# Performance work log

Measured on AMD Instinct MI355X. Metric: run time of the kernel, lower is better.

Reference implementation:

```python
import jax, jax.numpy as jnp
import numpy as np

B, N, IN_DIM = 2, 2048, 1024
DIM, DEPTH, HEADS, DH = 512, 4, 8, 128
INNER = HEADS * DH  # 1024
MLP, NCLS = 1024, 2
EPS = 1e-5


def setup_inputs() -> dict:
    key = jax.random.key(0)
    ks = jax.random.split(key, 10)
    r = lambda k, shape: (jax.random.normal(k, shape, dtype=jnp.float32) * 0.02)
    return {
        "x": jax.random.normal(ks[0], (B, N, IN_DIM), dtype=jnp.float32),
        "mask": jnp.ones((B, N), dtype=jnp.float32),
        "proj_w": r(ks[1], (IN_DIM, DIM)),
        "proj_b": jnp.zeros((DIM,), jnp.float32),
        "cls_token": jax.random.normal(ks[2], (1, 1, DIM), dtype=jnp.float32),
        "ln1_g": jnp.ones((DEPTH, DIM), jnp.float32),
        "ln1_b": jnp.zeros((DEPTH, DIM), jnp.float32),
        "qkv_w": r(ks[3], (DEPTH, DIM, 3 * INNER)),
        "out_w": r(ks[4], (DEPTH, INNER, DIM)),
        "out_b": jnp.zeros((DEPTH, DIM), jnp.float32),
        "ln2_g": jnp.ones((DEPTH, DIM), jnp.float32),
        "ln2_b": jnp.zeros((DEPTH, DIM), jnp.float32),
        "ff_w1": r(ks[5], (DEPTH, DIM, MLP)),
        "ff_b1": jnp.zeros((DEPTH, MLP), jnp.float32),
        "ff_w2": r(ks[6], (DEPTH, MLP, DIM)),
        "ff_b2": jnp.zeros((DEPTH, DIM), jnp.float32),
        "norm_g": jnp.ones((DIM,), jnp.float32),
        "norm_b": jnp.zeros((DIM,), jnp.float32),
        "head_ln_g": jnp.ones((DIM,), jnp.float32),
        "head_ln_b": jnp.zeros((DIM,), jnp.float32),
        "head_w": r(ks[7], (DIM, NCLS)),
        "head_b": jnp.zeros((NCLS,), jnp.float32),
    }


def _ln(x, g, b):
    m = jnp.mean(x, axis=-1, keepdims=True)
    v = jnp.mean((x - m) ** 2, axis=-1, keepdims=True)
    return (x - m) * jax.lax.rsqrt(v + EPS) * g + b


def reference(x, mask, proj_w, proj_b, cls_token, ln1_g, ln1_b, qkv_w, out_w,
              out_b, ln2_g, ln2_b, ff_w1, ff_b1, ff_w2, ff_b2, norm_g, norm_b,
              head_ln_g, head_ln_b, head_w, head_b):
    b = x.shape[0]
    scale = DH ** -0.5
    # input projection + ReLU
    h = jax.nn.relu(x @ proj_w + proj_b)  # [b, n, dim]
    # prepend cls token; extend mask with a 1 for it
    cls = jnp.broadcast_to(cls_token, (b, 1, DIM))
    h = jnp.concatenate([cls, h], axis=1)  # [b, n+1, dim]
    m_full = jnp.concatenate([jnp.ones((b, 1), mask.dtype), mask], axis=1)
    keep = (m_full != 0)[:, None, None, :]  # [b,1,1,n+1]

    for l in range(DEPTH):  # NOTE: original blocks have NO residual connections
        hn = _ln(h, ln1_g[l], ln1_b[l])
        qkv = hn @ qkv_w[l]  # [b, n+1, 3*inner]
        q, k, v = jnp.split(qkv, 3, axis=-1)
        resh = lambda t: t.reshape(b, -1, HEADS, DH).transpose(0, 2, 1, 3)
        q, k, v = resh(q), resh(k), resh(v)  # [b, h, n+1, dh]
        dots = jnp.einsum('bhid,bhjd->bhij', q, k) * scale
        dots = jnp.where(keep, dots, -jnp.inf)
        attn = jax.nn.softmax(dots, axis=-1)
        o = jnp.einsum('bhij,bhjd->bhid', attn, v)
        o = o.transpose(0, 2, 1, 3).reshape(b, -1, INNER)
        h = o @ out_w[l] + out_b[l]  # attention out (no residual)
        hn = _ln(h, ln2_g[l], ln2_b[l])
        h = jax.nn.gelu(hn @ ff_w1[l] + ff_b1[l], approximate=False) @ ff_w2[l] + ff_b2[l]

    pooled = h[:, 0]  # cls pooling
    pooled = _ln(pooled, norm_g, norm_b)
    pooled = _ln(pooled, head_ln_g, head_ln_b)
    return pooled @ head_w + head_b  # [b, num_classes]
```

## Files before the change

### kernel.cpp

```cpp
#include <hip/hip_runtime.h>
#include <hip/hip_bf16.h>
#include <stdint.h>

#define B_      2
#define N_      2048
#define S_      2049
#define SP_     2176
#define MP_     (B_*SP_)
#define IN_DIM_ 1024
#define DIM_    512
#define HEADS_  8
#define DH_     128
#define INNER_  1024
#define MLP_    1024
#define DEPTH_  4
#define NKV_    (SP_/64)
#define NCHUNK_ 4
#define TPC_    9

typedef __bf16 bf16;
typedef __bf16 bf16x4 __attribute__((ext_vector_type(4)));
typedef __bf16 bf16x8 __attribute__((ext_vector_type(8)));
typedef float  f32x4  __attribute__((ext_vector_type(4)));

#define AS1 __attribute__((address_space(1)))
#define AS3 __attribute__((address_space(3)))
__device__ __forceinline__ void gload16(const bf16* g, bf16* l) {
    __builtin_amdgcn_global_load_lds((const AS1 void*)g, (AS3 void*)l, 16, 0, 0);
}

__global__ __launch_bounds__(256) void wconv_kernel(const float* __restrict__ src,
                                                    bf16* __restrict__ dst,
                                                    int K, int N)
{
    __shared__ float tile[32][33];
    size_t mo = (size_t)blockIdx.z * K * N;
    int n0 = blockIdx.x * 32, k0 = blockIdx.y * 32;
    int tx = threadIdx.x & 31, ty = threadIdx.x >> 5;
#pragma unroll
    for (int i = 0; i < 32; i += 8)
        tile[ty + i][tx] = src[mo + (size_t)(k0 + ty + i) * N + n0 + tx];
    __syncthreads();
#pragma unroll
    for (int i = 0; i < 32; i += 8)
        dst[mo + (size_t)(n0 + ty + i) * K + k0 + tx] = (bf16)tile[tx][ty + i];
}

__global__ __launch_bounds__(256) void xconv_kernel(const float* __restrict__ x,
                                                    bf16* __restrict__ xb)
{
    int idx = blockIdx.x * 256 + threadIdx.x;
    int row = idx >> 7;
    int c   = (idx & 127) * 8;
    int b = row / SP_, s = row - b * SP_;
    bf16x8 v;
    if (s >= 1 && s <= N_) {
        const float* src = x + (size_t)(b * N_ + s - 1) * IN_DIM_ + c;
#pragma unroll
        for (int i = 0; i < 8; ++i) v[i] = (bf16)src[i];
    } else {
#pragma unroll
        for (int i = 0; i < 8; ++i) v[i] = (bf16)0.f;
    }
    *(bf16x8*)&xb[(size_t)row * IN_DIM_ + c] = v;
}

__global__ __launch_bounds__(256) void mask_kernel(const float* __restrict__ mask,
                                                   float* __restrict__ pb)
{
    int j = blockIdx.x * 256 + threadIdx.x;
    int b = blockIdx.y;
    if (j >= SP_) return;
    float v;
    if (j == 0) v = 0.f;
    else if (j <= N_) v = (mask[(size_t)b * N_ + j - 1] != 0.f) ? 0.f : -1e30f;
    else v = -1e30f;
    pb[(size_t)b * SP_ + j] = v;
}

__global__ void cls_kernel(const float* __restrict__ cls, float* __restrict__ h)
{
    h[(size_t)(blockIdx.x * SP_) * DIM_ + threadIdx.x] = cls[threadIdx.x];
}

__global__ __launch_bounds__(256) void ln_kernel(const float* __restrict__ h,
                                                 const float* __restrict__ g,
                                                 const float* __restrict__ bta,
                                                 bf16* __restrict__ out)
{
    int row  = blockIdx.x * 4 + (threadIdx.x >> 6);
    int lane = threadIdx.x & 63;
    const float* x = h + (size_t)row * DIM_;
    float v[8]; float s = 0.f;
#pragma unroll
    for (int i = 0; i < 8; ++i) { v[i] = x[lane + 64 * i]; s += v[i]; }
#pragma unroll
    for (int o = 32; o; o >>= 1) s += __shfl_xor(s, o);
    float mean = s * (1.f / DIM_);
    float vs = 0.f;
#pragma unroll
    for (int i = 0; i < 8; ++i) { float d = v[i] - mean; vs += d * d; }
#pragma unroll
    for (int o = 32; o; o >>= 1) vs += __shfl_xor(vs, o);
    float rstd = rsqrtf(vs * (1.f / DIM_) + 1e-5f);
    bf16* orow = out + (size_t)row * DIM_;
#pragma unroll
    for (int i = 0; i < 8; ++i)
        orow[lane + 64 * i] = (bf16)((v[i] - mean) * rstd * g[lane + 64 * i] + bta[lane + 64 * i]);
}

template<int BM, int BN, int ACT, int OUTBF>
__global__ __launch_bounds__(256) void gemm_bt(const bf16* __restrict__ A,
                                               const bf16* __restrict__ Bt,
                                               const float* __restrict__ bias,
                                               void* __restrict__ Cp,
                                               int M, int N, int K)
{
    constexpr int MF = (BM == 128) ? 4 : ((BN == 128) ? 4 : 2);
    constexpr int NF = (BM == 128) ? 4 : 2;
    constexpr int AT = BM / 32, BT = BN / 32;
    __shared__ __align__(16) bf16 As[BM * 64];
    __shared__ __align__(16) bf16 Bs[BN * 64];
    const int tid  = threadIdx.x;
    const int wave = tid >> 6, lane = tid & 63;
    const int bm = blockIdx.x * BM, bn = blockIdx.y * BN;
    const int wr = (BM == 128) ? (wave >> 1) * 64 : ((BN == 64) ? (wave >> 1) * 32 : 0);
    const int wc = (BM == 128) ? (wave & 1) * 64 : ((BN == 64) ? (wave & 1) * 32 : wave * 32);
    const int fr = lane & 15, fk = (lane >> 4) * 8;
    const int gr = lane >> 3, gc = (lane & 7) * 8;

    f32x4 acc[MF][NF];
#pragma unroll
    for (int m = 0; m < MF; ++m)
#pragma unroll
        for (int n = 0; n < NF; ++n) acc[m][n] = (f32x4){0.f, 0.f, 0.f, 0.f};

    for (int k0 = 0; k0 < K; k0 += 64) {
#pragma unroll
        for (int t = 0; t < AT; ++t) {
            int chunk = wave * AT + t;
            int r = chunk * 8 + gr;
            gload16(&A[(size_t)(bm + r) * K + k0 + (gc ^ ((r & 7) << 3))], &As[chunk * 512]);
        }
#pragma unroll
        for (int t = 0; t < BT; ++t) {
            int chunk = wave * BT + t;
            int r = chunk * 8 + gr;
            gload16(&Bt[(size_t)(bn + r) * K + k0 + (gc ^ ((r & 7) << 3))], &Bs[chunk * 512]);
        }
        __syncthreads();
#pragma unroll
        for (int kk = 0; kk < 2; ++kk) {
            bf16x8 af[MF], bb[NF];
#pragma unroll
            for (int m = 0; m < MF; ++m) {
                int r = wr + m * 16 + fr;
                af[m] = *(const bf16x8*)&As[r * 64 + ((kk * 32 + fk) ^ ((r & 7) << 3))];
            }
#pragma unroll
            for (int n = 0; n < NF; ++n) {
                int r = wc + n * 16 + fr;
                bb[n] = *(const bf16x8*)&Bs[r * 64 + ((kk * 32 + fk) ^ ((r & 7) << 3))];
            }
#pragma unroll
            for (int m = 0; m < MF; ++m)
#pragma unroll
                for (int n = 0; n < NF; ++n)
                    acc[m][n] = __builtin_amdgcn_mfma_f32_16x16x32_bf16(af[m], bb[n], acc[m][n], 0, 0, 0);
        }
        __syncthreads();
    }

    const int fc = lane & 15, fr4 = (lane >> 4) * 4;
#pragma unroll
    for (int n = 0; n < NF; ++n) {
        int col = bn + wc + n * 16 + fc;
        float bv = bias ? bias[col] : 0.f;
#pragma unroll
        for (int m = 0; m < MF; ++m) {
#pragma unroll
            for (int j = 0; j < 4; ++j) {
                int row = bm + wr + m * 16 + fr4 + j;
                float v = acc[m][n][j] + bv;
                if (ACT == 1) v = fmaxf(v, 0.f);
                if (ACT == 2) v = 0.5f * v * (1.f + erff(v * 0.70710678118654752f));
                if (OUTBF) ((bf16*)Cp)[(size_t)row * N + col] = (bf16)v;
                else       ((float*)Cp)[(size_t)row * N + col] = v;
            }
        }
    }
}

__global__ __launch_bounds__(256)
__attribute__((amdgpu_num_vgpr(168)))
void attn_kernel(const bf16* __restrict__ qkv,
                 const float* __restrict__ pb,
                 bf16* __restrict__ o0,
                 bf16* __restrict__ o1,
                 bf16* __restrict__ o2,
                 bf16* __restrict__ o3,
                 float* __restrict__ mlbuf)
{
    __shared__ __align__(16) bf16 Ks[64 * 128];
    __shared__ __align__(16) bf16 Vt[128 * 64];
    __shared__ __align__(16) bf16 Ps[4][32 * 64];

    const int bh = blockIdx.x, b = bh >> 3, hh = bh & 7;
    const int q0 = blockIdx.y * 128;
    const int chunk = blockIdx.z;
    const int t0 = chunk * TPC_;
    const int t1 = (t0 + TPC_ < NKV_) ? t0 + TPC_ : NKV_;
    bf16* obuf = (chunk == 0) ? o0 : (chunk == 1) ? o1 : (chunk == 2) ? o2 : o3;

    const int tid = threadIdx.x, wave = tid >> 6, lane = tid & 63;
    const int fc = lane & 15, g = lane >> 4, g8 = g * 8, rr0 = g * 4;
    bf16* Pw = &Ps[wave][0];

    const bf16* qb  = qkv + (size_t)(b * SP_) * (3 * INNER_) + hh * DH_;
    const bf16* kb  = qb + INNER_;
    const bf16* vb  = qb + 2 * INNER_;
    const float* pbb = pb + (size_t)b * SP_;

    bf16x8 aq[2][4];
#pragma unroll
    for (int m = 0; m < 2; ++m)
#pragma unroll
        for (int kk = 0; kk < 4; ++kk)
            aq[m][kk] = *(const bf16x8*)&qb[(size_t)(q0 + wave * 32 + m * 16 + fc) * (3 * INNER_) + kk * 32 + g8];

    f32x4 accO[2][8];
#pragma unroll
    for (int m = 0; m < 2; ++m)
#pragma unroll
        for (int f = 0; f < 8; ++f) accO[m][f] = (f32x4){0.f, 0.f, 0.f, 0.f};
    float mrow[2] = {-3e38f, -3e38f};
    float lrow[2] = {0.f, 0.f};
    const float scale = 0.08838834764831845f;

    auto issueK = [&](int kt) {
        int j0 = kt * 64;
#pragma unroll
        for (int t = 0; t < 4; ++t) {
            int ck = wave * 4 + t;
            int r = ck * 4 + (lane >> 4);
            int cp = (lane & 15) * 8;
            gload16(&kb[(size_t)(j0 + r) * (3 * INNER_) + (cp ^ ((r & 15) << 3))], &Ks[ck * 512]);
        }
    };
    const int vquad = tid >> 4;
    const int vd8   = (tid & 15) * 8;
    bf16x8 vreg[4];
    auto issueV = [&](int kt) {
        int j0 = kt * 64;
#pragma unroll
        for (int i = 0; i < 4; ++i)
            vreg[i] = *(const bf16x8*)&vb[(size_t)(j0 + vquad * 4 + i) * (3 * INNER_) + vd8];
    };

    issueK(t0);
    issueV(t0);
    for (int kt = t0; kt < t1; ++kt) {
        int j0 = kt * 64;
        __syncthreads();
#pragma unroll
        for (int di = 0; di < 8; ++di) {
            int rd = vd8 + di;
            bf16x4 w = { vreg[0][di], vreg[1][di], vreg[2][di], vreg[3][di] };
            *(bf16x4*)&Vt[rd * 64 + ((vquad * 4) ^ ((((rd & 7) ^ ((rd >> 3) & 7))) << 3))] = w;
        }
        __syncthreads();
        if (kt + 1 < t1) issueV(kt + 1);

        f32x4 sf[2][4];
#pragma unroll
        for (int m = 0; m < 2; ++m)
#pragma unroll
            for (int f = 0; f < 4; ++f) sf[m][f] = (f32x4){0.f, 0.f, 0.f, 0.f};
        __builtin_amdgcn_s_setprio(1);
#pragma unroll
        for (int kk = 0; kk < 4; ++kk) {
            bf16x8 bk[4];
#pragma unroll
            for (int f = 0; f < 4; ++f) {
                int r = f * 16 + fc;
                bk[f] = *(const bf16x8*)&Ks[r * 128 + ((kk * 32 + g8) ^ ((r & 15) << 3))];
            }
#pragma unroll
            for (int m = 0; m < 2; ++m)
#pragma unroll
                for (int f = 0; f < 4; ++f)
                    sf[m][f] = __builtin_amdgcn_mfma_f32_16x16x32_bf16(bk[f], aq[m][kk], sf[m][f], 0, 0, 0);
        }
        __builtin_amdgcn_s_setprio(0);
        __syncthreads();
        if (kt + 1 < t1) issueK(kt + 1);

        float rmax[2] = {-3e38f, -3e38f};
#pragma unroll
        for (int f = 0; f < 4; ++f) {
            f32x4 mb = *(const f32x4*)&pbb[j0 + f * 16 + rr0];
#pragma unroll
            for (int m = 0; m < 2; ++m)
#pragma unroll
                for (int r = 0; r < 4; ++r) {
                    float s = sf[m][f][r] * scale + mb[r];
                    sf[m][f][r] = s;
                    rmax[m] = fmaxf(rmax[m], s);
                }
        }
#pragma unroll
        for (int m = 0; m < 2; ++m) {
            rmax[m] = fmaxf(rmax[m], __shfl_xor(rmax[m], 16));
            rmax[m] = fmaxf(rmax[m], __shfl_xor(rmax[m], 32));
            if (__any(rmax[m] > mrow[m] + 5.f)) {
                float mn = fmaxf(mrow[m], rmax[m]);
                float corr = __expf(mrow[m] - mn);
                mrow[m] = mn;
                lrow[m] *= corr;
                float c0 = __shfl(corr, rr0 + 0);
                float c1 = __shfl(corr, rr0 + 1);
                float c2 = __shfl(corr, rr0 + 2);
                float c3 = __shfl(corr, rr0 + 3);
#pragma unroll
                for (int f = 0; f < 8; ++f) {
                    accO[m][f][0] *= c0; accO[m][f][1] *= c1;
                    accO[m][f][2] *= c2; accO[m][f][3] *= c3;
                }
            }
        }
#pragma unroll
        for (int m = 0; m < 2; ++m)
#pragma unroll
            for (int f = 0; f < 4; ++f) {
                bf16x4 pw;
#pragma unroll
                for (int r = 0; r < 4; ++r) {
                    float p = __expf(sf[m][f][r] - mrow[m]);
                    lrow[m] += p;
                    pw[r] = (bf16)p;
                }
                int rq = m * 16 + fc;
                *(bf16x4*)&Pw[rq * 64 + ((f * 16 + rr0) ^ ((rq & 7) << 3))] = pw;
            }
        __builtin_amdgcn_s_setprio(1);
#pragma unroll
        for (int kk = 0; kk < 2; ++kk) {
            bf16x8 ap[2];
#pragma unroll
            for (int m = 0; m < 2; ++m) {
                int rq = m * 16 + fc;
                ap[m] = *(const bf16x8*)&Pw[rq * 64 + ((kk * 32 + g8) ^ ((rq & 7) << 3))];
            }
#pragma unroll
            for (int f = 0; f < 8; ++f) {
                int rd = f * 16 + fc;
                bf16x8 bv = *(const bf16x8*)&Vt[rd * 64 + ((kk * 32 + g8) ^ ((((rd & 7) ^ ((rd >> 3) & 7))) << 3))];
#pragma unroll
                for (int m = 0; m < 2; ++m)
                    accO[m][f] = __builtin_amdgcn_mfma_f32_16x16x32_bf16(ap[m], bv, accO[m][f], 0, 0, 0);
            }
        }
        __builtin_amdgcn_s_setprio(0);
    }

#pragma unroll
    for (int m = 0; m < 2; ++m) {
        float l = lrow[m];
        l += __shfl_xor(l, 16);
        l += __shfl_xor(l, 32);
        if (g == 0) {
            int q = q0 + wave * 32 + m * 16 + fc;
            size_t mi = ((size_t)(chunk * B_ * HEADS_ + bh) * SP_ + q) * 2;
            mlbuf[mi + 0] = mrow[m];
            mlbuf[mi + 1] = l;
        }
        float linv = (l > 0.f) ? 1.f / l : 0.f;
        float l0 = __shfl(linv, rr0 + 0);
        float l1 = __shfl(linv, rr0 + 1);
        float l2 = __shfl(linv, rr0 + 2);
        float l3 = __shfl(linv, rr0 + 3);
#pragma unroll
        for (int f = 0; f < 8; ++f) {
            int col = hh * DH_ + f * 16 + fc;
            size_t base = (size_t)(b * SP_ + q0 + wave * 32 + m * 16 + rr0) * INNER_ + col;
            obuf[base + 0 * INNER_] = (bf16)(accO[m][f][0] * l0);
            obuf[base + 1 * INNER_] = (bf16)(accO[m][f][1] * l1);
            obuf[base + 2 * INNER_] = (bf16)(accO[m][f][2] * l2);
            obuf[base + 3 * INNER_] = (bf16)(accO[m][f][3] * l3);
        }
    }
}

__global__ __launch_bounds__(256) void attn_combine_kernel(const bf16* __restrict__ o0,
                                                           const bf16* __restrict__ o1,
                                                           const bf16* __restrict__ o2,
                                                           bf16* __restrict__ o3,
                                                           const float* __restrict__ mlbuf)
{
    const int bh = blockIdx.y, b = bh >> 3, hh = bh & 7;
    int gx = blockIdx.x * 256 + threadIdx.x;
    int q  = gx >> 4;
    int d  = (gx & 15) * 8;

    float mv[NCHUNK_], lv[NCHUNK_];
#pragma unroll
    for (int c = 0; c < NCHUNK_; ++c) {
        size_t mi = ((size_t)(c * B_ * HEADS_ + bh) * SP_ + q) * 2;
        mv[c] = mlbuf[mi];
        lv[c] = mlbuf[mi + 1];
    }
    float M = mv[0];
#pragma unroll
    for (int c = 1; c < NCHUNK_; ++c) M = fmaxf(M, mv[c]);
    float w[NCHUNK_], den = 0.f;
#pragma unroll
    for (int c = 0; c < NCHUNK_; ++c) { w[c] = lv[c] * __expf(mv[c] - M); den += w[c]; }
    float r = (den > 0.f) ? 1.f / den : 0.f;

    size_t base = (size_t)(b * SP_ + q) * INNER_ + hh * DH_ + d;
    bf16x8 v0 = *(const bf16x8*)&o0[base];
    bf16x8 v1 = *(const bf16x8*)&o1[base];
    bf16x8 v2 = *(const bf16x8*)&o2[base];
    bf16x8 v3 = *(const bf16x8*)&o3[base];
    bf16x8 out;
#pragma unroll
    for (int i = 0; i < 8; ++i)
        out[i] = (bf16)((w[0] * (float)v0[i] + w[1] * (float)v1[i]
                       + w[2] * (float)v2[i] + w[3] * (float)v3[i]) * r);
    *(bf16x8*)&o3[base] = out;
}

__global__ __launch_bounds__(64) void head_kernel(const float* __restrict__ h,
                                                  const float* __restrict__ ng, const float* __restrict__ nb,
                                                  const float* __restrict__ hg, const float* __restrict__ hb,
                                                  const float* __restrict__ hw, const float* __restrict__ hbi,
                                                  float* __restrict__ out)
{
    int b = blockIdx.x, lane = threadIdx.x;
    const float* xr = h + (size_t)(b * SP_) * DIM_;
    float v[8]; float s = 0.f;
#pragma unroll
    for (int i = 0; i < 8; ++i) { v[i] = xr[lane + 64 * i]; s += v[i]; }
#pragma unroll
    for (int o = 32; o; o >>= 1) s += __shfl_xor(s, o);
    float mean = s * (1.f / DIM_); float vs = 0.f;
#pragma unroll
    for (int i = 0; i < 8; ++i) { float d = v[i] - mean; vs += d * d; }
#pragma unroll
    for (int o = 32; o; o >>= 1) vs += __shfl_xor(vs, o);
    float rstd = rsqrtf(vs * (1.f / DIM_) + 1e-5f);
#pragma unroll
    for (int i = 0; i < 8; ++i) v[i] = (v[i] - mean) * rstd * ng[lane + 64 * i] + nb[lane + 64 * i];
    s = 0.f;
#pragma unroll
    for (int i = 0; i < 8; ++i) s += v[i];
#pragma unroll
    for (int o = 32; o; o >>= 1) s += __shfl_xor(s, o);
    mean = s * (1.f / DIM_); vs = 0.f;
#pragma unroll
    for (int i = 0; i < 8; ++i) { float d = v[i] - mean; vs += d * d; }
#pragma unroll
    for (int o = 32; o; o >>= 1) vs += __shfl_xor(vs, o);
    rstd = rsqrtf(vs * (1.f / DIM_) + 1e-5f);
#pragma unroll
    for (int i = 0; i < 8; ++i) v[i] = (v[i] - mean) * rstd * hg[lane + 64 * i] + hb[lane + 64 * i];
    float a0 = 0.f, a1 = 0.f;
#pragma unroll
    for (int i = 0; i < 8; ++i) {
        a0 += v[i] * hw[(lane + 64 * i) * 2 + 0];
        a1 += v[i] * hw[(lane + 64 * i) * 2 + 1];
    }
#pragma unroll
    for (int o = 32; o; o >>= 1) { a0 += __shfl_xor(a0, o); a1 += __shfl_xor(a1, o); }
    if (lane == 0) { out[b * 2 + 0] = a0 + hbi[0]; out[b * 2 + 1] = a1 + hbi[1]; }
}

extern "C" void kernel_launch(void* const* d_in, const int* in_sizes, int n_in,
                              void* d_out, int out_size, void* d_ws, size_t ws_size,
                              hipStream_t stream)
{
    const float* x       = (const float*)d_in[0];
    const float* mask    = (const float*)d_in[1];
    const float* proj_w  = (const float*)d_in[2];
    const float* proj_b  = (const float*)d_in[3];
    const float* cls_tok = (const float*)d_in[4];
    const float* ln1_g   = (const float*)d_in[5];
    const float* ln1_b   = (const float*)d_in[6];
    const float* qkv_w   = (const float*)d_in[7];
    const float* out_w   = (const float*)d_in[8];
    const float* out_b   = (const float*)d_in[9];
    const float* ln2_g   = (const float*)d_in[10];
    const float* ln2_b   = (const float*)d_in[11];
    const float* ff_w1   = (const float*)d_in[12];
    const float* ff_b1   = (const float*)d_in[13];
    const float* ff_w2   = (const float*)d_in[14];
    const float* ff_b2   = (const float*)d_in[15];
    const float* norm_g  = (const float*)d_in[16];
    const float* norm_b  = (const float*)d_in[17];
    const float* hln_g   = (const float*)d_in[18];
    const float* hln_b   = (const float*)d_in[19];
    const float* head_w  = (const float*)d_in[20];
    const float* head_b  = (const float*)d_in[21];

    char* p = (char*)d_ws;
    auto alloc = [&](size_t bytes) { char* r = p; p += (bytes + 255) & ~(size_t)255; return r; };
    bf16*  x_bf    = (bf16*)alloc((size_t)MP_ * IN_DIM_ * 2);
    float* h       = (float*)alloc((size_t)MP_ * DIM_ * 4);
    bf16*  hn_bf   = (bf16*)alloc((size_t)MP_ * DIM_ * 2);
    bf16*  qkv_bf  = (bf16*)alloc((size_t)MP_ * 3 * INNER_ * 2);
    bf16*  o_bf    = (bf16*)alloc((size_t)MP_ * INNER_ * 2);
    bf16*  ff1_bf  = (bf16*)alloc((size_t)MP_ * MLP_ * 2);
    bf16*  proj_wt = (bf16*)alloc((size_t)DIM_ * IN_DIM_ * 2);
    bf16*  qkv_wt  = (bf16*)alloc((size_t)DEPTH_ * 3 * INNER_ * DIM_ * 2);
    bf16*  out_wt  = (bf16*)alloc((size_t)DEPTH_ * DIM_ * INNER_ * 2);
    bf16*  ff1_wt  = (bf16*)alloc((size_t)DEPTH_ * MLP_ * DIM_ * 2);
    bf16*  ff2_wt  = (bf16*)alloc((size_t)DEPTH_ * DIM_ * MLP_ * 2);
    float* pbias   = (float*)alloc((size_t)B_ * SP_ * 4);
    if ((size_t)(p - (char*)d_ws) > ws_size) return;
    float* mlbuf = (float*)hn_bf;

    wconv_kernel<<<dim3(DIM_ / 32, IN_DIM_ / 32, 1), 256, 0, stream>>>(proj_w, proj_wt, IN_DIM_, DIM_);
    wconv_kernel<<<dim3(3 * INNER_ / 32, DIM_ / 32, DEPTH_), 256, 0, stream>>>(qkv_w, qkv_wt, DIM_, 3 * INNER_);
    wconv_kernel<<<dim3(DIM_ / 32, INNER_ / 32, DEPTH_), 256, 0, stream>>>(out_w, out_wt, INNER_, DIM_);
    wconv_kernel<<<dim3(MLP_ / 32, DIM_ / 32, DEPTH_), 256, 0, stream>>>(ff_w1, ff1_wt, DIM_, MLP_);
    wconv_kernel<<<dim3(DIM_ / 32, MLP_ / 32, DEPTH_), 256, 0, stream>>>(ff_w2, ff2_wt, MLP_, DIM_);

    xconv_kernel<<<MP_ * IN_DIM_ / 8 / 256, 256, 0, stream>>>(x, x_bf);
    mask_kernel<<<dim3((SP_ + 255) / 256, B_), 256, 0, stream>>>(mask, pbias);

    gemm_bt<64, 64, 1, 0><<<dim3(MP_ / 64, DIM_ / 64), 256, 0, stream>>>(x_bf, proj_wt, proj_b, h, MP_, DIM_, IN_DIM_);
    cls_kernel<<<B_, DIM_, 0, stream>>>(cls_tok, h);

    for (int l = 0; l < DEPTH_; ++l) {
        ln_kernel<<<MP_ / 4, 256, 0, stream>>>(h, ln1_g + l * DIM_, ln1_b + l * DIM_, hn_bf);
        gemm_bt<128, 128, 0, 1><<<dim3(MP_ / 128, 3 * INNER_ / 128), 256, 0, stream>>>(
            hn_bf, qkv_wt + (size_t)l * 3 * INNER_ * DIM_, nullptr, qkv_bf, MP_, 3 * INNER_, DIM_);
        attn_kernel<<<dim3(B_ * HEADS_, SP_ / 128, NCHUNK_), 256, 0, stream>>>(
            qkv_bf, pbias, x_bf, ff1_bf, (bf16*)h, o_bf, mlbuf);
        attn_combine_kernel<<<dim3(SP_ * 16 / 256, B_ * HEADS_), 256, 0, stream>>>(
            x_bf, ff1_bf, (const bf16*)h, o_bf, mlbuf);
        gemm_bt<64, 64, 0, 0><<<dim3(MP_ / 64, DIM_ / 64), 256, 0, stream>>>(
            o_bf, out_wt + (size_t)l * DIM_ * INNER_, out_b + l * DIM_, h, MP_, DIM_, INNER_);
        ln_kernel<<<MP_ / 4, 256, 0, stream>>>(h, ln2_g + l * DIM_, ln2_b + l * DIM_, hn_bf);
        gemm_bt<64, 128, 2, 1><<<dim3(MP_ / 64, MLP_ / 128), 256, 0, stream>>>(
            hn_bf, ff1_wt + (size_t)l * MLP_ * DIM_, ff_b1 + l * MLP_, ff1_bf, MP_, MLP_, DIM_);
        gemm_bt<64, 64, 0, 0><<<dim3(MP_ / 64, DIM_ / 64), 256, 0, stream>>>(
            ff1_bf, ff2_wt + (size_t)l * DIM_ * MLP_, ff_b2 + l * DIM_, h, MP_, DIM_, MLP_);
    }

    head_kernel<<<B_, 64, 0, stream>>>(h, norm_g, norm_b, hln_g, hln_b, head_w, head_b, (float*)d_out);
}
```

Before: 824.1 us.

## Double-buffer K and V tiles in attention kernel with one barrier per iteration

After: 868.5 us. 5.4% more time.

```diff
diff --git a/kernel.cpp b/kernel.cpp
--- a/kernel.cpp
+++ b/kernel.cpp
@@ -201,8 +201,8 @@
                  bf16* __restrict__ o3,
                  float* __restrict__ mlbuf)
 {
-    __shared__ __align__(16) bf16 Ks[64 * 128];
-    __shared__ __align__(16) bf16 Vt[128 * 64];
+    __shared__ __align__(16) bf16 Ks[2][64 * 128];
+    __shared__ __align__(16) bf16 Vt[2][128 * 64];
     __shared__ __align__(16) bf16 Ps[4][32 * 64];
 
     const int bh = blockIdx.x, b = bh >> 3, hh = bh & 7;
@@ -237,14 +237,14 @@
     float lrow[2] = {0.f, 0.f};
     const float scale = 0.08838834764831845f;
 
-    auto issueK = [&](int kt) {
+    auto issueK = [&](int kt, int buf) {
         int j0 = kt * 64;
 #pragma unroll
         for (int t = 0; t < 4; ++t) {
             int ck = wave * 4 + t;
             int r = ck * 4 + (lane >> 4);
             int cp = (lane & 15) * 8;
-            gload16(&kb[(size_t)(j0 + r) * (3 * INNER_) + (cp ^ ((r & 15) << 3))], &Ks[ck * 512]);
+            gload16(&kb[(size_t)(j0 + r) * (3 * INNER_) + (cp ^ ((r & 15) << 3))], &Ks[buf][ck * 512]);
         }
     };
     const int vquad = tid >> 4;
@@ -256,20 +256,29 @@
         for (int i = 0; i < 4; ++i)
             vreg[i] = *(const bf16x8*)&vb[(size_t)(j0 + vquad * 4 + i) * (3 * INNER_) + vd8];
     };
-
-    issueK(t0);
+    auto stageV = [&](int buf) {
+#pragma unroll
+        for (int di = 0; di < 8; ++di) {
+            int rd = vd8 + di;
+            bf16x4 w = { vreg[0][di], vreg[1][di], vreg[2][di], vreg[3][di] };
+            *(bf16x4*)&Vt[buf][rd * 64 + ((vquad * 4) ^ ((((rd & 7) ^ ((rd >> 3) & 7))) << 3))] = w;
+        }
+    };
+
     issueV(t0);
+    issueK(t0, 0);
+    stageV(0);
+    int cur = 0;
+
     for (int kt = t0; kt < t1; ++kt) {
         int j0 = kt * 64;
         __syncthreads();
-#pragma unroll
-        for (int di = 0; di < 8; ++di) {
-            int rd = vd8 + di;
-            bf16x4 w = { vreg[0][di], vreg[1][di], vreg[2][di], vreg[3][di] };
-            *(bf16x4*)&Vt[rd * 64 + ((vquad * 4) ^ ((((rd & 7) ^ ((rd >> 3) & 7))) << 3))] = w;
-        }
-        __syncthreads();
-        if (kt + 1 < t1) issueV(kt + 1);
+        int nxt = cur ^ 1;
+        bool more = (kt + 1 < t1);
+        if (more) {
+            issueV(kt + 1);
+            issueK(kt + 1, nxt);
+        }
 
         f32x4 sf[2][4];
 #pragma unroll
@@ -283,7 +292,7 @@
 #pragma unroll
             for (int f = 0; f < 4; ++f) {
                 int r = f * 16 + fc;
-                bk[f] = *(const bf16x8*)&Ks[r * 128 + ((kk * 32 + g8) ^ ((r & 15) << 3))];
+                bk[f] = *(const bf16x8*)&Ks[cur][r * 128 + ((kk * 32 + g8) ^ ((r & 15) << 3))];
             }
 #pragma unroll
             for (int m = 0; m < 2; ++m)
@@ -292,8 +301,8 @@
                     sf[m][f] = __builtin_amdgcn_mfma_f32_16x16x32_bf16(bk[f], aq[m][kk], sf[m][f], 0, 0, 0);
         }
         __builtin_amdgcn_s_setprio(0);
-        __syncthreads();
-        if (kt + 1 < t1) issueK(kt + 1);
+
+        if (more) stageV(nxt);
 
         float rmax[2] = {-3e38f, -3e38f};
 #pragma unroll
@@ -354,13 +363,14 @@
 #pragma unroll
             for (int f = 0; f < 8; ++f) {
                 int rd = f * 16 + fc;
-                bf16x8 bv = *(const bf16x8*)&Vt[rd * 64 + ((kk * 32 + g8) ^ ((((rd & 7) ^ ((rd >> 3) & 7))) << 3))];
+                bf16x8 bv = *(const bf16x8*)&Vt[cur][rd * 64 + ((kk * 32 + g8) ^ ((((rd & 7) ^ ((rd >> 3) & 7))) << 3))];
 #pragma unroll
                 for (int m = 0; m < 2; ++m)
                     accO[m][f] = __builtin_amdgcn_mfma_f32_16x16x32_bf16(ap[m], bv, accO[m][f], 0, 0, 0);
             }
         }
         __builtin_amdgcn_s_setprio(0);
+        cur = nxt;
     }
 
 #pragma unroll
```
